# Optimization experiments

Hardware: AMD Instinct MI355X
Metric: run time of the kernel (lower is better)

## Reference

```python
import jax, jax.numpy as jnp
import numpy as np

ALPHA = 0.2   # LeakyReLU negative slope
EPS = 1e-8
N_NODES = 100000
N_EDGES = 1600000
D_IN = 128
D_OUT = 128


def setup_inputs() -> dict:
    key = jax.random.key(0)
    k1, k2, k3, k4, k5 = jax.random.split(key, 5)
    h = jax.random.normal(k1, (N_NODES, D_IN), dtype=jnp.float32)
    edge_index = jax.random.randint(k2, (2, N_EDGES), 0, N_NODES, dtype=jnp.int32)
    edge_weight = jax.random.uniform(k3, (N_EDGES,), dtype=jnp.float32)
    # xavier-ish scaled params
    W = jax.random.normal(k4, (D_OUT, D_IN), dtype=jnp.float32) * (1.0 / np.sqrt(D_IN))
    a = jax.random.normal(k5, (1, 2 * D_OUT), dtype=jnp.float32) * (1.0 / np.sqrt(2 * D_OUT))
    return {"h": h, "edge_index": edge_index, "edge_weight": edge_weight, "W": W, "a": a}


def reference(h, edge_index, edge_weight, W, a):
    num_nodes = h.shape[0]
    Wh = h @ W.T                                   # [N, D_OUT]
    src, dst = edge_index[0], edge_index[1]
    d_out = Wh.shape[1]
    a_src = a[0, :d_out]                           # a^T [Wh_i || Wh_j] split into two dots
    a_dst = a[0, d_out:]
    Wh_src = Wh[src]                               # [E, D_OUT] edge gather
    e = Wh_src @ a_src + Wh[dst] @ a_dst           # [E]
    e = jnp.where(e >= 0, e, ALPHA * e)            # LeakyReLU
    e = e * edge_weight
    # segment softmax over edges sharing dst; torch init-to-zero amax => max(seg_max, 0)
    seg_max = jax.ops.segment_max(e, dst, num_segments=num_nodes)
    seg_max = jnp.maximum(seg_max, 0.0)
    ex = jnp.exp(e - seg_max[dst])
    seg_sum = jax.ops.segment_sum(ex, dst, num_segments=num_nodes)
    att = ex / (seg_sum[dst] + EPS)                # [E]
    # weighted scatter-add aggregation (dropout is identity in eval/p=0)
    h_prime = jax.ops.segment_sum(att[:, None] * Wh_src, dst, num_segments=num_nodes)
    return h_prime
```

## Files before the change

### kernel.cpp

```cpp
#include <hip/hip_runtime.h>
#include <hip/hip_bf16.h>
#include <math.h>

#define D_FEAT 128
#define ALPHA 0.2f
#define EPS 1e-8f

#define BSHIFT 7
#define BNODES 128
#define NB_MAX 800
#define NB_PAD 1024
#define CAP_B 2432
#define CCHUNK 2048

typedef __bf16 bf16x8 __attribute__((ext_vector_type(8)));
typedef float f32x4 __attribute__((ext_vector_type(4)));

__device__ __forceinline__ void split_bf16(const float* __restrict__ p,
                                           bf16x8& hi, bf16x8& lo)
{
    f32x4 a = *(const f32x4*)p;
    f32x4 b = *(const f32x4*)(p + 4);
#pragma unroll
    for (int j = 0; j < 4; ++j) {
        float x = a[j]; __bf16 xh = (__bf16)x;
        hi[j] = xh; lo[j] = (__bf16)(x - (float)xh);
        float y = b[j]; __bf16 yh = (__bf16)y;
        hi[j + 4] = yh; lo[j + 4] = (__bf16)(y - (float)yh);
    }
}

__global__ __launch_bounds__(256) void presplit_w(
    const float* __restrict__ W, __bf16* __restrict__ Whi, __bf16* __restrict__ Wlo)
{
    const int i = blockIdx.x * 256 + threadIdx.x;
    const float x = W[i];
    const __bf16 xh = (__bf16)x;
    Whi[i] = xh;
    Wlo[i] = (__bf16)(x - (float)xh);
}

__global__ __launch_bounds__(256) void gemm_s_kernel(
    const float* __restrict__ h,
    const __bf16* __restrict__ Whi, const __bf16* __restrict__ Wlo,
    const float* __restrict__ a, __bf16* __restrict__ Whb,
    float* __restrict__ s_src, float* __restrict__ s_dst, int N)
{
    const int wave = threadIdx.x >> 6;
    const int lane = threadIdx.x & 63;
    const int row0 = blockIdx.x * 64 + wave * 16;
    if (row0 >= N) return;

    const int l15 = lane & 15;
    const int quad = lane >> 4;

    int arow = row0 + l15;
    if (arow >= N) arow = N - 1;
    bf16x8 ahi[4], alo[4];
#pragma unroll
    for (int kk = 0; kk < 4; ++kk)
        split_bf16(h + (size_t)arow * D_FEAT + kk * 32 + quad * 8, ahi[kk], alo[kk]);

    f32x4 acc[8];
#pragma unroll
    for (int n = 0; n < 8; ++n) acc[n] = (f32x4){0.f, 0.f, 0.f, 0.f};

#pragma unroll
    for (int kk = 0; kk < 4; ++kk) {
#pragma unroll
        for (int n = 0; n < 8; ++n) {
            const size_t boff = (size_t)(n * 16 + l15) * D_FEAT + kk * 32 + quad * 8;
            const bf16x8 bhi = *(const bf16x8*)(Whi + boff);
            const bf16x8 blo = *(const bf16x8*)(Wlo + boff);
            acc[n] = __builtin_amdgcn_mfma_f32_16x16x32_bf16(ahi[kk], bhi, acc[n], 0, 0, 0);
            acc[n] = __builtin_amdgcn_mfma_f32_16x16x32_bf16(ahi[kk], blo, acc[n], 0, 0, 0);
            acc[n] = __builtin_amdgcn_mfma_f32_16x16x32_bf16(alo[kk], bhi, acc[n], 0, 0, 0);
        }
    }

    float psrc[4] = {0.f, 0.f, 0.f, 0.f};
    float pdst[4] = {0.f, 0.f, 0.f, 0.f};
#pragma unroll
    for (int n = 0; n < 8; ++n) {
        const int col = n * 16 + l15;
        const float as = a[col];
        const float ad = a[D_FEAT + col];
#pragma unroll
        for (int r = 0; r < 4; ++r) {
            const int row = row0 + quad * 4 + r;
            const float v = acc[n][r];
            if (row < N) Whb[(size_t)row * D_FEAT + col] = (__bf16)v;
            psrc[r] += v * as;
            pdst[r] += v * ad;
        }
    }
#pragma unroll
    for (int off = 1; off < 16; off <<= 1) {
#pragma unroll
        for (int r = 0; r < 4; ++r) {
            psrc[r] += __shfl_xor(psrc[r], off, 64);
            pdst[r] += __shfl_xor(pdst[r], off, 64);
        }
    }
    if (l15 == 0) {
#pragma unroll
        for (int r = 0; r < 4; ++r) {
            const int row = row0 + quad * 4 + r;
            if (row < N) { s_src[row] = psrc[r]; s_dst[row] = pdst[r]; }
        }
    }
}

__global__ __launch_bounds__(256) void bin_sort_local(
    const int* __restrict__ src, const int* __restrict__ dst,
    const float* __restrict__ ew,
    const float* __restrict__ s_src, const float* __restrict__ s_dst,
    int* __restrict__ gcur, uint2* __restrict__ bin, int E, int NB)
{
    __shared__ uint2 srt[CCHUNK];
    __shared__ unsigned short sbkt[CCHUNK];
    __shared__ int lhist[NB_PAD];
    __shared__ int loff[NB_PAD];
    __shared__ int lcur[NB_PAD];
    __shared__ int gbase[NB_PAD];
    __shared__ int sh[256];

    const int t = threadIdx.x;
    const int i0 = blockIdx.x * CCHUNK + t * 8;

    lhist[t] = 0; lhist[t + 256] = 0; lhist[t + 512] = 0; lhist[t + 768] = 0;
    __syncthreads();

    int n = E - i0; n = n < 0 ? 0 : (n > 8 ? 8 : n);
    int ss[8], dd[8];
    float wwv[8], exv[8];
    unsigned meta[8];
    int bb[8];

    if (n == 8) {
        const int4 sa = *(const int4*)(src + i0);
        const int4 sb = *(const int4*)(src + i0 + 4);
        const int4 da = *(const int4*)(dst + i0);
        const int4 db = *(const int4*)(dst + i0 + 4);
        const float4 wa = *(const float4*)(ew + i0);
        const float4 wb = *(const float4*)(ew + i0 + 4);
        ss[0] = sa.x; ss[1] = sa.y; ss[2] = sa.z; ss[3] = sa.w;
        ss[4] = sb.x; ss[5] = sb.y; ss[6] = sb.z; ss[7] = sb.w;
        dd[0] = da.x; dd[1] = da.y; dd[2] = da.z; dd[3] = da.w;
        dd[4] = db.x; dd[5] = db.y; dd[6] = db.z; dd[7] = db.w;
        wwv[0] = wa.x; wwv[1] = wa.y; wwv[2] = wa.z; wwv[3] = wa.w;
        wwv[4] = wb.x; wwv[5] = wb.y; wwv[6] = wb.z; wwv[7] = wb.w;
    } else {
        for (int k = 0; k < n; ++k) {
            ss[k] = src[i0 + k]; dd[k] = dst[i0 + k]; wwv[k] = ew[i0 + k];
        }
    }
#pragma unroll
    for (int k = 0; k < 8; ++k) {
        if (k < n) {
            const int s = ss[k], d = dd[k];
            float e = s_src[s] + s_dst[d];
            e = (e >= 0.f) ? e : ALPHA * e;
            e *= wwv[k];
            exv[k] = expf(e);
            bb[k] = d >> BSHIFT;
            meta[k] = (unsigned)s | ((unsigned)(d & (BNODES - 1)) << 17);
            atomicAdd(&lhist[bb[k]], 1);
        }
    }
    __syncthreads();

    const int v0 = lhist[4 * t];
    const int v1 = lhist[4 * t + 1];
    const int v2 = lhist[4 * t + 2];
    const int v3 = lhist[4 * t + 3];
    const int ts = v0 + v1 + v2 + v3;
    sh[t] = ts;
    __syncthreads();
    for (int off = 1; off < 256; off <<= 1) {
        int x = (t >= off) ? sh[t - off] : 0;
        __syncthreads();
        sh[t] += x;
        __syncthreads();
    }
    int run = sh[t] - ts;
    loff[4 * t] = run;     lcur[4 * t] = run;     run += v0;
    loff[4 * t + 1] = run; lcur[4 * t + 1] = run; run += v1;
    loff[4 * t + 2] = run; lcur[4 * t + 2] = run; run += v2;
    loff[4 * t + 3] = run; lcur[4 * t + 3] = run;
    const int total = sh[255];

    for (int b = t; b < NB; b += 256) {
        const int c = lhist[b];
        gbase[b] = c ? atomicAdd(&gcur[b], c) : 0;
    }
    __syncthreads();

#pragma unroll
    for (int k = 0; k < 8; ++k) {
        if (k < n) {
            const int p = atomicAdd(&lcur[bb[k]], 1);
            srt[p] = make_uint2(meta[k], __float_as_uint(exv[k]));
            sbkt[p] = (unsigned short)bb[k];
        }
    }
    __syncthreads();

    for (int i = t; i < total; i += 256) {
        const int b = sbkt[i];
        const int gpos = gbase[b] + (i - loff[b]);
        if (gpos < CAP_B)
            bin[(size_t)b * CAP_B + gpos] = srt[i];
    }
}

__global__ __launch_bounds__(512) void sort_aggregate(
    const int* __restrict__ gcur, const uint2* __restrict__ bin,
    const __bf16* __restrict__ Whb, float* __restrict__ out, int N)
{
    __shared__ uint2 srec[CAP_B];
    __shared__ int lhist[BNODES];
    __shared__ int loff[BNODES];
    __shared__ int lcur[BNODES];
    __shared__ int sh[BNODES];

    const int t = threadIdx.x;
    const int b = blockIdx.x;
    const size_t base = (size_t)b * CAP_B;
    const int node0 = b << BSHIFT;
    const int nnodes = min(BNODES, N - node0);
    int cnt = gcur[b];
    if (cnt > CAP_B) cnt = CAP_B;

    if (t < BNODES) lhist[t] = 0;
    __syncthreads();

    for (int i = t; i < cnt; i += 512)
        atomicAdd(&lhist[(bin[base + i].x >> 17) & (BNODES - 1)], 1);
    __syncthreads();

    int hv = 0;
    if (t < BNODES) { hv = lhist[t]; sh[t] = hv; }
    __syncthreads();
    for (int off = 1; off < BNODES; off <<= 1) {
        int x = (t >= off && t < BNODES) ? sh[t - off] : 0;
        __syncthreads();
        if (t < BNODES) sh[t] += x;
        __syncthreads();
    }
    if (t < BNODES) { loff[t] = sh[t] - hv; lcur[t] = sh[t] - hv; }
    __syncthreads();

    for (int i = t; i < cnt; i += 512) {
        const uint2 r = bin[base + i];
        const unsigned dl = (r.x >> 17) & (BNODES - 1);
        const int p = atomicAdd(&lcur[dl], 1);
        srec[p] = make_uint2(r.x & 0x1FFFFu, r.y);
    }
    __syncthreads();

    const int wave = t >> 6;
    const int lane = t & 63;
    const int quad = lane >> 4;
    const int c0 = (lane & 15) * 8;

    for (int nd = wave; nd < nnodes; nd += 8) {
        const int rb = loff[nd];
        const int cnt_n = lhist[nd];

        float ssum = 0.f;
        for (int jj = lane; jj < cnt_n; jj += 64)
            ssum += __uint_as_float(srec[rb + jj].y);
#pragma unroll
        for (int off = 1; off < 64; off <<= 1)
            ssum += __shfl_xor(ssum, off, 64);
        const float inv = 1.f / (ssum + EPS);

        float acc[8];
#pragma unroll
        for (int i = 0; i < 8; ++i) acc[i] = 0.f;

        int j = 0;
        for (; j + 7 < cnt_n; j += 8) {
            const uint2 m0 = srec[rb + j + quad];
            const uint2 m1 = srec[rb + j + 4 + quad];
            const float a0 = __uint_as_float(m0.y) * inv;
            const float a1 = __uint_as_float(m1.y) * inv;
            const bf16x8 v0 = *(const bf16x8*)(Whb + (size_t)m0.x * D_FEAT + c0);
            const bf16x8 v1 = *(const bf16x8*)(Whb + (size_t)m1.x * D_FEAT + c0);
#pragma unroll
            for (int i = 0; i < 8; ++i)
                acc[i] += a0 * (float)v0[i] + a1 * (float)v1[i];
        }
        for (; j < cnt_n; j += 4) {
            const int je = j + quad;
            const int jc = je < cnt_n ? je : cnt_n - 1;
            const uint2 m = srec[rb + jc];
            const float a0 = (je < cnt_n) ? __uint_as_float(m.y) * inv : 0.f;
            const bf16x8 v = *(const bf16x8*)(Whb + (size_t)m.x * D_FEAT + c0);
#pragma unroll
            for (int i = 0; i < 8; ++i) acc[i] += a0 * (float)v[i];
        }
#pragma unroll
        for (int i = 0; i < 8; ++i) {
            acc[i] += __shfl_xor(acc[i], 16, 64);
            acc[i] += __shfl_xor(acc[i], 32, 64);
        }
        if (lane < 16) {
            f32x4 r0, r1;
            r0[0] = acc[0]; r0[1] = acc[1]; r0[2] = acc[2]; r0[3] = acc[3];
            r1[0] = acc[4]; r1[1] = acc[5]; r1[2] = acc[6]; r1[3] = acc[7];
            float* po = out + (size_t)(node0 + nd) * D_FEAT + c0;
            *(f32x4*)po = r0;
            *(f32x4*)(po + 4) = r1;
        }
    }
}

extern "C" void kernel_launch(void* const* d_in, const int* in_sizes, int n_in,
                              void* d_out, int out_size, void* d_ws, size_t ws_size,
                              hipStream_t stream) {
    const float* h  = (const float*)d_in[0];
    const int* eidx = (const int*)d_in[1];
    const float* ew = (const float*)d_in[2];
    const float* W  = (const float*)d_in[3];
    const float* a  = (const float*)d_in[4];
    float* out      = (float*)d_out;

    const int N = in_sizes[0] / D_FEAT;
    const int E = in_sizes[2];
    const int* src = eidx;
    const int* dst = eidx + E;

    const int NB = (N + BNODES - 1) / BNODES;

    char* ws = (char*)d_ws;
    size_t off = 0;
    int*    gcur      = (int*)(ws + off);   off += (size_t)NB_MAX * 4;
    float*  s_src     = (float*)(ws + off); off += (size_t)N * 4;
    float*  s_dst     = (float*)(ws + off); off += (size_t)N * 4;
    off = (off + 15) & ~(size_t)15;
    __bf16* Whi       = (__bf16*)(ws + off); off += (size_t)D_FEAT * D_FEAT * 2;
    __bf16* Wlo       = (__bf16*)(ws + off); off += (size_t)D_FEAT * D_FEAT * 2;
    uint2*  bin       = (uint2*)(ws + off);  off += (size_t)NB_MAX * CAP_B * 8;
    __bf16* Whb       = (__bf16*)(ws + off); off += (size_t)N * D_FEAT * 2;

    hipMemsetAsync(gcur, 0, (size_t)NB * 4, stream);

    presplit_w<<<64, 256, 0, stream>>>(W, Whi, Wlo);
    gemm_s_kernel<<<(N + 63) / 64, 256, 0, stream>>>(h, Whi, Wlo, a, Whb, s_src, s_dst, N);
    bin_sort_local<<<(E + CCHUNK - 1) / CCHUNK, 256, 0, stream>>>(
        src, dst, ew, s_src, s_dst, gcur, bin, E, NB);
    sort_aggregate<<<NB, 512, 0, stream>>>(gcur, bin, Whb, out, N);
}
```

Measured before the change: 286.2 us.

## Coarsen edge bins to 256 nodes and double GEMM rows per wave

The binning pass now groups edges into 256-node coarse bins, which halves the number of buckets and shrinks the local histogram and scan work in bin_sort_local. The aggregate kernel launches two blocks per coarse bin, and each block filters out the half of the records belonging to its own 128 nodes. The GEMM kernel now computes 32 rows per wave instead of 16, reusing each W fragment load across two row tiles. The cost is that each aggregate block reads its whole coarse bin twice and discards half of it, and the GEMM uses more registers.

```diff
diff --git a/kernel.cpp b/kernel.cpp
--- a/kernel.cpp
+++ b/kernel.cpp
@@ -6,11 +6,12 @@
 #define ALPHA 0.2f
 #define EPS 1e-8f
 
-#define BSHIFT 7
-#define BNODES 128
-#define NB_MAX 800
-#define NB_PAD 1024
-#define CAP_B 2432
+#define BSHIFT 8
+#define BNODES 256
+#define NBC_MAX 400
+#define NB_PAD 512
+#define CAP_B 4608
+#define CAP_F 2432
 #define CCHUNK 2048
 
 typedef __bf16 bf16x8 __attribute__((ext_vector_type(8)));
@@ -48,22 +49,28 @@
 {
     const int wave = threadIdx.x >> 6;
     const int lane = threadIdx.x & 63;
-    const int row0 = blockIdx.x * 64 + wave * 16;
+    const int row0 = blockIdx.x * 128 + wave * 32;
     if (row0 >= N) return;
 
     const int l15 = lane & 15;
     const int quad = lane >> 4;
 
-    int arow = row0 + l15;
-    if (arow >= N) arow = N - 1;
-    bf16x8 ahi[4], alo[4];
-#pragma unroll
-    for (int kk = 0; kk < 4; ++kk)
-        split_bf16(h + (size_t)arow * D_FEAT + kk * 32 + quad * 8, ahi[kk], alo[kk]);
-
-    f32x4 acc[8];
-#pragma unroll
-    for (int n = 0; n < 8; ++n) acc[n] = (f32x4){0.f, 0.f, 0.f, 0.f};
+    bf16x8 ahi[2][4], alo[2][4];
+#pragma unroll
+    for (int m = 0; m < 2; ++m) {
+        int arow = row0 + m * 16 + l15;
+        if (arow >= N) arow = N - 1;
+#pragma unroll
+        for (int kk = 0; kk < 4; ++kk)
+            split_bf16(h + (size_t)arow * D_FEAT + kk * 32 + quad * 8,
+                       ahi[m][kk], alo[m][kk]);
+    }
+
+    f32x4 acc[2][8];
+#pragma unroll
+    for (int m = 0; m < 2; ++m)
+#pragma unroll
+        for (int n = 0; n < 8; ++n) acc[m][n] = (f32x4){0.f, 0.f, 0.f, 0.f};
 
 #pragma unroll
     for (int kk = 0; kk < 4; ++kk) {
@@ -72,41 +79,48 @@
             const size_t boff = (size_t)(n * 16 + l15) * D_FEAT + kk * 32 + quad * 8;
             const bf16x8 bhi = *(const bf16x8*)(Whi + boff);
             const bf16x8 blo = *(const bf16x8*)(Wlo + boff);
-            acc[n] = __builtin_amdgcn_mfma_f32_16x16x32_bf16(ahi[kk], bhi, acc[n], 0, 0, 0);
-            acc[n] = __builtin_amdgcn_mfma_f32_16x16x32_bf16(ahi[kk], blo, acc[n], 0, 0, 0);
-            acc[n] = __builtin_amdgcn_mfma_f32_16x16x32_bf16(alo[kk], bhi, acc[n], 0, 0, 0);
-        }
-    }
-
-    float psrc[4] = {0.f, 0.f, 0.f, 0.f};
-    float pdst[4] = {0.f, 0.f, 0.f, 0.f};
-#pragma unroll
-    for (int n = 0; n < 8; ++n) {
-        const int col = n * 16 + l15;
-        const float as = a[col];
-        const float ad = a[D_FEAT + col];
-#pragma unroll
-        for (int r = 0; r < 4; ++r) {
-            const int row = row0 + quad * 4 + r;
-            const float v = acc[n][r];
-            if (row < N) Whb[(size_t)row * D_FEAT + col] = (__bf16)v;
-            psrc[r] += v * as;
-            pdst[r] += v * ad;
-        }
-    }
-#pragma unroll
-    for (int off = 1; off < 16; off <<= 1) {
-#pragma unroll
-        for (int r = 0; r < 4; ++r) {
-            psrc[r] += __shfl_xor(psrc[r], off, 64);
-            pdst[r] += __shfl_xor(pdst[r], off, 64);
-        }
-    }
-    if (l15 == 0) {
-#pragma unroll
-        for (int r = 0; r < 4; ++r) {
-            const int row = row0 + quad * 4 + r;
-            if (row < N) { s_src[row] = psrc[r]; s_dst[row] = pdst[r]; }
+#pragma unroll
+            for (int m = 0; m < 2; ++m) {
+                acc[m][n] = __builtin_amdgcn_mfma_f32_16x16x32_bf16(ahi[m][kk], bhi, acc[m][n], 0, 0, 0);
+                acc[m][n] = __builtin_amdgcn_mfma_f32_16x16x32_bf16(ahi[m][kk], blo, acc[m][n], 0, 0, 0);
+                acc[m][n] = __builtin_amdgcn_mfma_f32_16x16x32_bf16(alo[m][kk], bhi, acc[m][n], 0, 0, 0);
+            }
+        }
+    }
+
+#pragma unroll
+    for (int m = 0; m < 2; ++m) {
+        const int rbase = row0 + m * 16;
+        float psrc[4] = {0.f, 0.f, 0.f, 0.f};
+        float pdst[4] = {0.f, 0.f, 0.f, 0.f};
+#pragma unroll
+        for (int n = 0; n < 8; ++n) {
+            const int col = n * 16 + l15;
+            const float as = a[col];
+            const float ad = a[D_FEAT + col];
+#pragma unroll
+            for (int r = 0; r < 4; ++r) {
+                const int row = rbase + quad * 4 + r;
+                const float v = acc[m][n][r];
+                if (row < N) Whb[(size_t)row * D_FEAT + col] = (__bf16)v;
+                psrc[r] += v * as;
+                pdst[r] += v * ad;
+            }
+        }
+#pragma unroll
+        for (int off = 1; off < 16; off <<= 1) {
+#pragma unroll
+            for (int r = 0; r < 4; ++r) {
+                psrc[r] += __shfl_xor(psrc[r], off, 64);
+                pdst[r] += __shfl_xor(pdst[r], off, 64);
+            }
+        }
+        if (l15 == 0) {
+#pragma unroll
+            for (int r = 0; r < 4; ++r) {
+                const int row = rbase + quad * 4 + r;
+                if (row < N) { s_src[row] = psrc[r]; s_dst[row] = pdst[r]; }
+            }
         }
     }
 }
@@ -128,7 +142,7 @@
     const int t = threadIdx.x;
     const int i0 = blockIdx.x * CCHUNK + t * 8;
 
-    lhist[t] = 0; lhist[t + 256] = 0; lhist[t + 512] = 0; lhist[t + 768] = 0;
+    lhist[t] = 0; lhist[t + 256] = 0;
     __syncthreads();
 
     int n = E - i0; n = n < 0 ? 0 : (n > 8 ? 8 : n);
@@ -170,11 +184,9 @@
     }
     __syncthreads();
 
-    const int v0 = lhist[4 * t];
-    const int v1 = lhist[4 * t + 1];
-    const int v2 = lhist[4 * t + 2];
-    const int v3 = lhist[4 * t + 3];
-    const int ts = v0 + v1 + v2 + v3;
+    const int v0 = lhist[2 * t];
+    const int v1 = lhist[2 * t + 1];
+    const int ts = v0 + v1;
     sh[t] = ts;
     __syncthreads();
     for (int off = 1; off < 256; off <<= 1) {
@@ -184,10 +196,8 @@
         __syncthreads();
     }
     int run = sh[t] - ts;
-    loff[4 * t] = run;     lcur[4 * t] = run;     run += v0;
-    loff[4 * t + 1] = run; lcur[4 * t + 1] = run; run += v1;
-    loff[4 * t + 2] = run; lcur[4 * t + 2] = run; run += v2;
-    loff[4 * t + 3] = run; lcur[4 * t + 3] = run;
+    loff[2 * t] = run;     lcur[2 * t] = run;     run += v0;
+    loff[2 * t + 1] = run; lcur[2 * t + 1] = run;
     const int total = sh[255];
 
     for (int b = t; b < NB; b += 256) {
@@ -218,44 +228,50 @@
     const int* __restrict__ gcur, const uint2* __restrict__ bin,
     const __bf16* __restrict__ Whb, float* __restrict__ out, int N)
 {
-    __shared__ uint2 srec[CAP_B];
-    __shared__ int lhist[BNODES];
-    __shared__ int loff[BNODES];
-    __shared__ int lcur[BNODES];
-    __shared__ int sh[BNODES];
+    __shared__ uint2 srec[CAP_F];
+    __shared__ int lhist[128];
+    __shared__ int loff[128];
+    __shared__ int lcur[128];
+    __shared__ int sh[128];
 
     const int t = threadIdx.x;
-    const int b = blockIdx.x;
-    const size_t base = (size_t)b * CAP_B;
-    const int node0 = b << BSHIFT;
-    const int nnodes = min(BNODES, N - node0);
-    int cnt = gcur[b];
+    const int fb = blockIdx.x;
+    const int bc = fb >> 1;
+    const int hb = fb & 1;
+    const size_t base = (size_t)bc * CAP_B;
+    const int node0 = fb << 7;
+    const int nnodes = min(128, N - node0);
+    int cnt = gcur[bc];
     if (cnt > CAP_B) cnt = CAP_B;
 
-    if (t < BNODES) lhist[t] = 0;
-    __syncthreads();
-
-    for (int i = t; i < cnt; i += 512)
-        atomicAdd(&lhist[(bin[base + i].x >> 17) & (BNODES - 1)], 1);
+    if (t < 128) lhist[t] = 0;
+    __syncthreads();
+
+    for (int i = t; i < cnt; i += 512) {
+        const unsigned dl8 = (bin[base + i].x >> 17) & 255u;
+        if ((int)(dl8 >> 7) == hb) atomicAdd(&lhist[dl8 & 127u], 1);
+    }
     __syncthreads();
 
     int hv = 0;
-    if (t < BNODES) { hv = lhist[t]; sh[t] = hv; }
-    __syncthreads();
-    for (int off = 1; off < BNODES; off <<= 1) {
-        int x = (t >= off && t < BNODES) ? sh[t - off] : 0;
+    if (t < 128) { hv = lhist[t]; sh[t] = hv; }
+    __syncthreads();
+    for (int off = 1; off < 128; off <<= 1) {
+        int x = (t >= off && t < 128) ? sh[t - off] : 0;
         __syncthreads();
-        if (t < BNODES) sh[t] += x;
+        if (t < 128) sh[t] += x;
         __syncthreads();
     }
-    if (t < BNODES) { loff[t] = sh[t] - hv; lcur[t] = sh[t] - hv; }
+    if (t < 128) { loff[t] = sh[t] - hv; lcur[t] = sh[t] - hv; }
     __syncthreads();
 
     for (int i = t; i < cnt; i += 512) {
         const uint2 r = bin[base + i];
-        const unsigned dl = (r.x >> 17) & (BNODES - 1);
-        const int p = atomicAdd(&lcur[dl], 1);
-        srec[p] = make_uint2(r.x & 0x1FFFFu, r.y);
+        const unsigned dl8 = (r.x >> 17) & 255u;
+        if ((int)(dl8 >> 7) == hb) {
+            const int p = atomicAdd(&lcur[dl8 & 127u], 1);
+            if (p < CAP_F) srec[p] = make_uint2(r.x & 0x1FFFFu, r.y);
+        }
     }
     __syncthreads();
 
@@ -266,7 +282,8 @@
 
     for (int nd = wave; nd < nnodes; nd += 8) {
         const int rb = loff[nd];
-        const int cnt_n = lhist[nd];
+        int cnt_n = lhist[nd];
+        if (rb + cnt_n > CAP_F) cnt_n = (CAP_F > rb) ? CAP_F - rb : 0;
 
         float ssum = 0.f;
         for (int jj = lane; jj < cnt_n; jj += 64)
@@ -332,24 +349,25 @@
     const int* src = eidx;
     const int* dst = eidx + E;
 
-    const int NB = (N + BNODES - 1) / BNODES;
+    const int NBC = (N + BNODES - 1) / BNODES;
+    const int NBF = 2 * NBC;
 
     char* ws = (char*)d_ws;
     size_t off = 0;
-    int*    gcur      = (int*)(ws + off);   off += (size_t)NB_MAX * 4;
+    int*    gcur      = (int*)(ws + off);   off += (size_t)NBC_MAX * 4;
     float*  s_src     = (float*)(ws + off); off += (size_t)N * 4;
     float*  s_dst     = (float*)(ws + off); off += (size_t)N * 4;
     off = (off + 15) & ~(size_t)15;
     __bf16* Whi       = (__bf16*)(ws + off); off += (size_t)D_FEAT * D_FEAT * 2;
     __bf16* Wlo       = (__bf16*)(ws + off); off += (size_t)D_FEAT * D_FEAT * 2;
-    uint2*  bin       = (uint2*)(ws + off);  off += (size_t)NB_MAX * CAP_B * 8;
+    uint2*  bin       = (uint2*)(ws + off);  off += (size_t)NBC_MAX * CAP_B * 8;
     __bf16* Whb       = (__bf16*)(ws + off); off += (size_t)N * D_FEAT * 2;
 
-    hipMemsetAsync(gcur, 0, (size_t)NB * 4, stream);
+    hipMemsetAsync(gcur, 0, (size_t)NBC * 4, stream);
 
     presplit_w<<<64, 256, 0, stream>>>(W, Whi, Wlo);
-    gemm_s_kernel<<<(N + 63) / 64, 256, 0, stream>>>(h, Whi, Wlo, a, Whb, s_src, s_dst, N);
+    gemm_s_kernel<<<(N + 127) / 128, 256, 0, stream>>>(h, Whi, Wlo, a, Whb, s_src, s_dst, N);
     bin_sort_local<<<(E + CCHUNK - 1) / CCHUNK, 256, 0, stream>>>(
-        src, dst, ew, s_src, s_dst, gcur, bin, E, NB);
-    sort_aggregate<<<NB, 512, 0, stream>>>(gcur, bin, Whb, out, N);
-}
+        src, dst, ew, s_src, s_dst, gcur, bin, E, NBC);
+    sort_aggregate<<<NBF, 512, 0, stream>>>(gcur, bin, Whb, out, N);
+}
```

After: 289.0 us. About the same (+1.0%).

## Double GEMM rows per wave and restructure aggregation with shared softmax sums

Applied to the files above, without the earlier changes.

The GEMM kernel now processes 32 rows per wave (two 16-row M tiles), so each loaded W fragment feeds twice as many MFMAs and half as many blocks are launched. In the aggregation kernel, per-node softmax denominators are accumulated with shared-memory float atomics during the bucket scatter, which removes the separate per-node reduction pass. Normalization is applied once after the cross-lane reduction, and a 16-edge unrolled loop issues four independent row gathers at once to raise memory-level parallelism. The costs are higher register pressure in both kernels and shared-memory atomic contention on the sums.

```diff
diff --git a/kernel.cpp b/kernel.cpp
--- a/kernel.cpp
+++ b/kernel.cpp
@@ -48,22 +48,28 @@
 {
     const int wave = threadIdx.x >> 6;
     const int lane = threadIdx.x & 63;
-    const int row0 = blockIdx.x * 64 + wave * 16;
+    const int row0 = blockIdx.x * 128 + wave * 32;
     if (row0 >= N) return;
 
     const int l15 = lane & 15;
     const int quad = lane >> 4;
 
-    int arow = row0 + l15;
-    if (arow >= N) arow = N - 1;
-    bf16x8 ahi[4], alo[4];
-#pragma unroll
-    for (int kk = 0; kk < 4; ++kk)
-        split_bf16(h + (size_t)arow * D_FEAT + kk * 32 + quad * 8, ahi[kk], alo[kk]);
-
-    f32x4 acc[8];
-#pragma unroll
-    for (int n = 0; n < 8; ++n) acc[n] = (f32x4){0.f, 0.f, 0.f, 0.f};
+    bf16x8 ahi[2][4], alo[2][4];
+#pragma unroll
+    for (int m = 0; m < 2; ++m) {
+        int arow = row0 + m * 16 + l15;
+        if (arow >= N) arow = N - 1;
+#pragma unroll
+        for (int kk = 0; kk < 4; ++kk)
+            split_bf16(h + (size_t)arow * D_FEAT + kk * 32 + quad * 8,
+                       ahi[m][kk], alo[m][kk]);
+    }
+
+    f32x4 acc[2][8];
+#pragma unroll
+    for (int m = 0; m < 2; ++m)
+#pragma unroll
+        for (int n = 0; n < 8; ++n) acc[m][n] = (f32x4){0.f, 0.f, 0.f, 0.f};
 
 #pragma unroll
     for (int kk = 0; kk < 4; ++kk) {
@@ -72,41 +78,48 @@
             const size_t boff = (size_t)(n * 16 + l15) * D_FEAT + kk * 32 + quad * 8;
             const bf16x8 bhi = *(const bf16x8*)(Whi + boff);
             const bf16x8 blo = *(const bf16x8*)(Wlo + boff);
-            acc[n] = __builtin_amdgcn_mfma_f32_16x16x32_bf16(ahi[kk], bhi, acc[n], 0, 0, 0);
-            acc[n] = __builtin_amdgcn_mfma_f32_16x16x32_bf16(ahi[kk], blo, acc[n], 0, 0, 0);
-            acc[n] = __builtin_amdgcn_mfma_f32_16x16x32_bf16(alo[kk], bhi, acc[n], 0, 0, 0);
-        }
-    }
-
-    float psrc[4] = {0.f, 0.f, 0.f, 0.f};
-    float pdst[4] = {0.f, 0.f, 0.f, 0.f};
-#pragma unroll
-    for (int n = 0; n < 8; ++n) {
-        const int col = n * 16 + l15;
-        const float as = a[col];
-        const float ad = a[D_FEAT + col];
-#pragma unroll
-        for (int r = 0; r < 4; ++r) {
-            const int row = row0 + quad * 4 + r;
-            const float v = acc[n][r];
-            if (row < N) Whb[(size_t)row * D_FEAT + col] = (__bf16)v;
-            psrc[r] += v * as;
-            pdst[r] += v * ad;
-        }
-    }
-#pragma unroll
-    for (int off = 1; off < 16; off <<= 1) {
-#pragma unroll
-        for (int r = 0; r < 4; ++r) {
-            psrc[r] += __shfl_xor(psrc[r], off, 64);
-            pdst[r] += __shfl_xor(pdst[r], off, 64);
-        }
-    }
-    if (l15 == 0) {
-#pragma unroll
-        for (int r = 0; r < 4; ++r) {
-            const int row = row0 + quad * 4 + r;
-            if (row < N) { s_src[row] = psrc[r]; s_dst[row] = pdst[r]; }
+#pragma unroll
+            for (int m = 0; m < 2; ++m) {
+                acc[m][n] = __builtin_amdgcn_mfma_f32_16x16x32_bf16(ahi[m][kk], bhi, acc[m][n], 0, 0, 0);
+                acc[m][n] = __builtin_amdgcn_mfma_f32_16x16x32_bf16(ahi[m][kk], blo, acc[m][n], 0, 0, 0);
+                acc[m][n] = __builtin_amdgcn_mfma_f32_16x16x32_bf16(alo[m][kk], bhi, acc[m][n], 0, 0, 0);
+            }
+        }
+    }
+
+#pragma unroll
+    for (int m = 0; m < 2; ++m) {
+        const int rbase = row0 + m * 16;
+        float psrc[4] = {0.f, 0.f, 0.f, 0.f};
+        float pdst[4] = {0.f, 0.f, 0.f, 0.f};
+#pragma unroll
+        for (int n = 0; n < 8; ++n) {
+            const int col = n * 16 + l15;
+            const float as = a[col];
+            const float ad = a[D_FEAT + col];
+#pragma unroll
+            for (int r = 0; r < 4; ++r) {
+                const int row = rbase + quad * 4 + r;
+                const float v = acc[m][n][r];
+                if (row < N) Whb[(size_t)row * D_FEAT + col] = (__bf16)v;
+                psrc[r] += v * as;
+                pdst[r] += v * ad;
+            }
+        }
+#pragma unroll
+        for (int off = 1; off < 16; off <<= 1) {
+#pragma unroll
+            for (int r = 0; r < 4; ++r) {
+                psrc[r] += __shfl_xor(psrc[r], off, 64);
+                pdst[r] += __shfl_xor(pdst[r], off, 64);
+            }
+        }
+        if (l15 == 0) {
+#pragma unroll
+            for (int r = 0; r < 4; ++r) {
+                const int row = rbase + quad * 4 + r;
+                if (row < N) { s_src[row] = psrc[r]; s_dst[row] = pdst[r]; }
+            }
         }
     }
 }
@@ -219,6 +232,7 @@
     const __bf16* __restrict__ Whb, float* __restrict__ out, int N)
 {
     __shared__ uint2 srec[CAP_B];
+    __shared__ float ssums[BNODES];
     __shared__ int lhist[BNODES];
     __shared__ int loff[BNODES];
     __shared__ int lcur[BNODES];
@@ -232,7 +246,7 @@
     int cnt = gcur[b];
     if (cnt > CAP_B) cnt = CAP_B;
 
-    if (t < BNODES) lhist[t] = 0;
+    if (t < BNODES) { lhist[t] = 0; ssums[t] = 0.f; }
     __syncthreads();
 
     for (int i = t; i < cnt; i += 512)
@@ -256,6 +270,7 @@
         const unsigned dl = (r.x >> 17) & (BNODES - 1);
         const int p = atomicAdd(&lcur[dl], 1);
         srec[p] = make_uint2(r.x & 0x1FFFFu, r.y);
+        atomicAdd(&ssums[dl], __uint_as_float(r.y));
     }
     __syncthreads();
 
@@ -267,25 +282,33 @@
     for (int nd = wave; nd < nnodes; nd += 8) {
         const int rb = loff[nd];
         const int cnt_n = lhist[nd];
-
-        float ssum = 0.f;
-        for (int jj = lane; jj < cnt_n; jj += 64)
-            ssum += __uint_as_float(srec[rb + jj].y);
-#pragma unroll
-        for (int off = 1; off < 64; off <<= 1)
-            ssum += __shfl_xor(ssum, off, 64);
-        const float inv = 1.f / (ssum + EPS);
+        const float inv = 1.f / (ssums[nd] + EPS);
 
         float acc[8];
 #pragma unroll
         for (int i = 0; i < 8; ++i) acc[i] = 0.f;
 
         int j = 0;
+        for (; j + 15 < cnt_n; j += 16) {
+            uint2 m[4];
+#pragma unroll
+            for (int g = 0; g < 4; ++g) m[g] = srec[rb + j + g * 4 + quad];
+            bf16x8 v[4];
+#pragma unroll
+            for (int g = 0; g < 4; ++g)
+                v[g] = *(const bf16x8*)(Whb + (size_t)m[g].x * D_FEAT + c0);
+#pragma unroll
+            for (int g = 0; g < 4; ++g) {
+                const float a0 = __uint_as_float(m[g].y);
+#pragma unroll
+                for (int i = 0; i < 8; ++i) acc[i] += a0 * (float)v[g][i];
+            }
+        }
         for (; j + 7 < cnt_n; j += 8) {
             const uint2 m0 = srec[rb + j + quad];
             const uint2 m1 = srec[rb + j + 4 + quad];
-            const float a0 = __uint_as_float(m0.y) * inv;
-            const float a1 = __uint_as_float(m1.y) * inv;
+            const float a0 = __uint_as_float(m0.y);
+            const float a1 = __uint_as_float(m1.y);
             const bf16x8 v0 = *(const bf16x8*)(Whb + (size_t)m0.x * D_FEAT + c0);
             const bf16x8 v1 = *(const bf16x8*)(Whb + (size_t)m1.x * D_FEAT + c0);
 #pragma unroll
@@ -296,7 +319,7 @@
             const int je = j + quad;
             const int jc = je < cnt_n ? je : cnt_n - 1;
             const uint2 m = srec[rb + jc];
-            const float a0 = (je < cnt_n) ? __uint_as_float(m.y) * inv : 0.f;
+            const float a0 = (je < cnt_n) ? __uint_as_float(m.y) : 0.f;
             const bf16x8 v = *(const bf16x8*)(Whb + (size_t)m.x * D_FEAT + c0);
 #pragma unroll
             for (int i = 0; i < 8; ++i) acc[i] += a0 * (float)v[i];
@@ -305,6 +328,7 @@
         for (int i = 0; i < 8; ++i) {
             acc[i] += __shfl_xor(acc[i], 16, 64);
             acc[i] += __shfl_xor(acc[i], 32, 64);
+            acc[i] *= inv;
         }
         if (lane < 16) {
             f32x4 r0, r1;
@@ -348,7 +372,7 @@
     hipMemsetAsync(gcur, 0, (size_t)NB * 4, stream);
 
     presplit_w<<<64, 256, 0, stream>>>(W, Whi, Wlo);
-    gemm_s_kernel<<<(N + 63) / 64, 256, 0, stream>>>(h, Whi, Wlo, a, Whb, s_src, s_dst, N);
+    gemm_s_kernel<<<(N + 127) / 128, 256, 0, stream>>>(h, Whi, Wlo, a, Whb, s_src, s_dst, N);
     bin_sort_local<<<(E + CCHUNK - 1) / CCHUNK, 256, 0, stream>>>(
         src, dst, ew, s_src, s_dst, gcur, bin, E, NB);
     sort_aggregate<<<NB, 512, 0, stream>>>(gcur, bin, Whb, out, N);
```

New measurement: 270.5 us. -5.5%, faster.
